# Performance work log

Measured on AMD Instinct MI355X. Metric: run time of the kernel, lower is better.

## Reference

```python
import jax, jax.numpy as jnp
import numpy as np

EPS = 1e-6  # torch.nn.CosineSimilarity eps


def _emb_sum(table, ids):
    # ids: (N, L) int -> (N, D): gather rows then sum over tokens (EmbeddingBag-sum)
    return table[ids].sum(axis=1)


def _cos_rows(q, M):
    # cosine similarity of vector q (D,) against each row of M (N, D), torch eps semantics:
    # dot / max(||a||*||b||, eps)
    num = M @ q
    den = jnp.maximum(jnp.linalg.norm(M, axis=1) * jnp.linalg.norm(q), EPS)
    return num / den


def setup_inputs() -> dict:
    key = jax.random.key(0)
    ks = jax.random.split(key, 10)
    V, D = 50000, 128
    N_MEM, N_CAND, N_PERS, L, LQ = 65536, 10000, 20, 20, 32
    return {
        "xs": jax.random.randint(ks[0], (1, LQ), 0, V, dtype=jnp.int32),
        "candidates": jax.random.randint(ks[1], (N_CAND, L), 0, V, dtype=jnp.int32),
        "persona": jax.random.randint(ks[2], (N_PERS, L), 0, V, dtype=jnp.int32),
        "keys": jax.random.randint(ks[3], (N_MEM, L), 0, V, dtype=jnp.int32),
        "values": jax.random.randint(ks[4], (N_MEM, L), 0, V, dtype=jnp.int32),
        "label": jax.random.randint(ks[5], (1, LQ), 0, V, dtype=jnp.int32),
        "shared_emb": jax.random.normal(ks[6], (V, D), dtype=jnp.float32),
        "cand_emb": jax.random.normal(ks[7], (V, D), dtype=jnp.float32),
        "R_W": jax.random.normal(ks[8], (D, D), dtype=jnp.float32) * (1.0 / np.sqrt(D)),
        "R2_W": jax.random.normal(ks[9], (D, D), dtype=jnp.float32) * (1.0 / np.sqrt(D)),
    }


def reference(xs, candidates, persona, keys, values, label, shared_emb, cand_emb, R_W, R2_W):
    enc_keys = _emb_sum(shared_emb, keys)        # (N_mem, D)
    enc_values = _emb_sum(shared_emb, values)    # (N_mem, D)
    enc_cands = _emb_sum(cand_emb, candidates)   # (N_cand, D)
    enc_pers = _emb_sum(shared_emb, persona)     # (N_pers, D)

    q = shared_emb[xs].sum(axis=1).reshape(-1)   # (D,)

    for W in (R_W, R2_W):  # loop is hardcoded to 2 hops in the source
        att = jax.nn.softmax(_cos_rows(q, enc_pers))          # (N_pers,)
        hop = (att[:, None] * enc_pers).sum(axis=0)           # (D,)
        q_plus = (q + hop) @ W.T                               # Linear no bias
        att = jax.nn.softmax(_cos_rows(q_plus, enc_keys))     # (N_mem,)
        hop = (att[:, None] * enc_values).sum(axis=0)         # (D,)
        q = (q_plus + hop) @ W.T

    preds = _cos_rows(q, enc_cands)  # (N_cand,)
    return preds
```

## Files before the change

kernel.cpp:

```cpp
#include <hip/hip_runtime.h>
#include <math.h>
#include <stdint.h>

#define D 128
#define EPS 1e-6f
typedef unsigned short u16;


__device__ __forceinline__ float wave_sum(float v) {
#pragma unroll
    for (int off = 32; off > 0; off >>= 1) v += __shfl_xor(v, off, 64);
    return v;
}
__device__ __forceinline__ float halfwave_sum(float v) {
#pragma unroll
    for (int off = 16; off > 0; off >>= 1) v += __shfl_xor(v, off, 32);
    return v;
}

__device__ __forceinline__ float bf2f(u16 h) {
    union { unsigned u; float f; } x;
    x.u = ((unsigned)h) << 16;
    return x.f;
}
__device__ __forceinline__ float bflo(unsigned u) { return bf2f((u16)(u & 0xffff)); }
__device__ __forceinline__ float bfhi(unsigned u) { return bf2f((u16)(u >> 16)); }
__device__ __forceinline__ u16 f2bf(float f) {
    union { float f; unsigned u; } x;
    x.f = f;
    unsigned u = x.u;
    return (u16)((u + 0x7fff + ((u >> 16) & 1)) >> 16);
}
__device__ __forceinline__ unsigned pack2(float a, float b) {
    return (unsigned)f2bf(a) | ((unsigned)f2bf(b) << 16);
}

__global__ void prep_k(const float* __restrict__ semb, u16* __restrict__ tbl,
                       int V, const int* __restrict__ pers, int NP,
                       const int* __restrict__ xs, int LQ,
                       float* __restrict__ enc_pers, float* __restrict__ pnorms,
                       float* __restrict__ st, int nbK) {
    const int tid = threadIdx.x;
    const int bid = blockIdx.x;
    if (bid < nbK) {
        const int n = V * 64;
        const int stride = nbK * 256;
        for (int i = bid * 256 + tid; i < n; i += stride) {
            const int v = i >> 6;
            const int c2 = i & 63;
            const float2 ab = *(const float2*)(semb + (long)v * D + 2 * c2);
            *(unsigned*)(tbl + (long)v * D + 2 * c2) = pack2(ab.x, ab.y);
        }
    } else {
        const int lane = tid & 63;
        const int half = lane >> 5;
        const int hl = lane & 31;
        const int w0 = (bid - nbK) * 4 + (tid >> 6);
        const int npr = NP + 1;
        const int npairs = (npr + 1) >> 1;
        for (int w = w0; w < npairs; w += 12) {
            const int row = 2 * w + half;
            const bool valid = row < npr;
            const int rowc = valid ? row : NP;
            const bool isq = (rowc == NP);
            const int* ids = isq ? xs : (pers + (long)rowc * 20);
            const int L = isq ? LQ : 20;
            int myid = 0;
            if (hl < L) myid = ids[hl];
            float4 acc = {0.f, 0.f, 0.f, 0.f};
            for (int t = 0; t < L; ++t) {
                const int idx = __shfl(myid, (half << 5) + t, 64);
                const float4 e = *(const float4*)(semb + (long)idx * D + 4 * hl);
                acc.x += e.x; acc.y += e.y; acc.z += e.z; acc.w += e.w;
            }
            if (valid) {
                float* outp = isq ? st : (enc_pers + (long)rowc * D);
                *(float4*)(outp + 4 * hl) = acc;
                float sq = acc.x * acc.x + acc.y * acc.y + acc.z * acc.z + acc.w * acc.w;
                sq = halfwave_sum(sq);
                if (hl == 0) {
                    if (isq) st[384] = sqrtf(sq);
                    else pnorms[rowc] = sqrtf(sq);
                }
            }
        }
    }
}

__device__ void persona_dev(const float* __restrict__ pers_rows,
                            const float* __restrict__ pnorms,
                            const float* __restrict__ W, float* __restrict__ st,
                            int NP, float* smem, int tid) {
    float* qsh = smem;
    float* qh = smem + 128;
    float* att = smem + 256;
    float* red = smem + 320;
    if (tid < D) qsh[tid] = st[tid];
    __syncthreads();
    if (tid < NP) {
        float dot = 0.f;
        const float* pr = pers_rows + (long)tid * D;
        for (int d2 = 0; d2 < D; ++d2) dot += pr[d2] * qsh[d2];
        att[tid] = dot / fmaxf(pnorms[tid] * st[384], EPS);
    }
    __syncthreads();
    if (tid == 0) {
        float m = -1e30f;
        for (int p = 0; p < NP; ++p) m = fmaxf(m, att[p]);
        float s = 0.f;
        for (int p = 0; p < NP; ++p) { att[p] = __expf(att[p] - m); s += att[p]; }
        float inv = 1.f / s;
        for (int p = 0; p < NP; ++p) att[p] *= inv;
    }
    __syncthreads();
    if (tid < D) {
        float h = 0.f;
        for (int p = 0; p < NP; ++p) h += att[p] * pers_rows[(long)p * D + tid];
        qh[tid] = qsh[tid] + h;
    }
    __syncthreads();
    float qp = 0.f;
    if (tid < D) {
        for (int d2 = 0; d2 < D; ++d2) qp += W[(long)tid * D + d2] * qh[d2];
        st[128 + tid] = qp;
    }
    float sq = wave_sum(qp * qp);
    if ((tid & 63) == 0 && tid < 128) red[tid >> 6] = sq;
    __syncthreads();
    if (tid == 0) st[385] = sqrtf(red[0] + red[1]);
    if (tid < D) st[256 + tid] = 0.f;
    if (tid == 0) st[386] = 0.f;
}

__global__ void kvp_k(const u16* __restrict__ tbl, const int* __restrict__ kids,
                      const int* __restrict__ vids, int N,
                      u16* __restrict__ vb, float* __restrict__ knorms,
                      const float* __restrict__ enc_pers,
                      const float* __restrict__ pnorms,
                      const float* __restrict__ RW, float* __restrict__ st,
                      int NP) {
    __shared__ float smem[336];
    const int tid = threadIdx.x;
    const int bid = blockIdx.x;
    if (bid == 0) {
        persona_dev(enc_pers, pnorms, RW, st, NP, smem, tid);
        return;
    }
    const int lane = tid & 63;
    const int half = lane >> 5;
    const int hl = lane & 31;
    const int ghw = ((bid - 1) * 256 + tid) >> 5;
    const int nhw = ((gridDim.x - 1) * 256) >> 5;
    for (int i = ghw; i < N; i += nhw) {
        int kid = 0, vid = 0;
        if (hl < 20) {
            kid = kids[(long)i * 20 + hl];
            vid = vids[(long)i * 20 + hl];
        }
        float k0 = 0.f, k1 = 0.f, k2 = 0.f, k3 = 0.f;
        float v0 = 0.f, v1 = 0.f, v2 = 0.f, v3 = 0.f;
#pragma unroll
        for (int t = 0; t < 20; ++t) {
            const int kj = __shfl(kid, (half << 5) + t, 64);
            const int vj = __shfl(vid, (half << 5) + t, 64);
            const ushort4 ke = *(const ushort4*)(tbl + (long)kj * D + 4 * hl);
            const ushort4 ve = *(const ushort4*)(tbl + (long)vj * D + 4 * hl);
            k0 += bf2f(ke.x); k1 += bf2f(ke.y); k2 += bf2f(ke.z); k3 += bf2f(ke.w);
            v0 += bf2f(ve.x); v1 += bf2f(ve.y); v2 += bf2f(ve.z); v3 += bf2f(ve.w);
        }
        uint2 pv;
        pv.x = pack2(v0, v1);
        pv.y = pack2(v2, v3);
        *(uint2*)(vb + (long)i * D + 4 * hl) = pv;
        float sq = halfwave_sum(k0 * k0 + k1 * k1 + k2 * k2 + k3 * k3);
        if (hl == 0) knorms[i] = sqrtf(sq);
    }
}

__global__ void a2_k(const u16* __restrict__ tbl, const float* __restrict__ st,
                     float* __restrict__ s, int V) {
    const int lane = threadIdx.x & 63;
    const float2 qp2 = *(const float2*)(st + 128 + 2 * lane);
    const int gw = (int)((blockIdx.x * blockDim.x + threadIdx.x) >> 6);
    const int nw = (int)((gridDim.x * blockDim.x) >> 6);
    for (int v = gw; v < V; v += nw) {
        const unsigned u = *(const unsigned*)(tbl + (long)v * D + 2 * lane);
        float d = bflo(u) * qp2.x + bfhi(u) * qp2.y;
        d = wave_sum(d);
        if (lane == 0) s[v] = d;
    }
}

__global__ void attcv_k(const float* __restrict__ sv, const int* __restrict__ kids,
                        const float* __restrict__ knorms, const u16* __restrict__ vb,
                        float* __restrict__ st, int N) {
    __shared__ float smem[129];
    const int tid = threadIdx.x;
    const int lane = tid & 63;
    const int half = lane >> 5;
    const int hl = lane & 31;
    const float qpn = st[385];
    const int ghw = (int)((blockIdx.x * blockDim.x + tid) >> 5);
    const int nhw = (int)((gridDim.x * blockDim.x) >> 5);
    float a0 = 0.f, a1 = 0.f, a2 = 0.f, a3 = 0.f;
    float esum = 0.f;
    for (int i = ghw; i < N; i += nhw) {
        float partial = 0.f;
        if (hl < 20) partial = sv[kids[(long)i * 20 + hl]];
        const float dot = halfwave_sum(partial);
        const float c = dot / fmaxf(knorms[i] * qpn, EPS);
        const float e = __expf(c);
        const uint2 vh = *(const uint2*)(vb + (long)i * D + 4 * hl);
        a0 += e * bflo(vh.x);
        a1 += e * bfhi(vh.x);
        a2 += e * bflo(vh.y);
        a3 += e * bfhi(vh.y);
        if (hl == 0) esum += e;
    }
    a0 += __shfl_xor(a0, 32, 64);
    a1 += __shfl_xor(a1, 32, 64);
    a2 += __shfl_xor(a2, 32, 64);
    a3 += __shfl_xor(a3, 32, 64);
    esum += __shfl_xor(esum, 32, 64);
    if (tid < 129) smem[tid] = 0.f;
    __syncthreads();
    if (half == 0) {
        atomicAdd(&smem[4 * hl + 0], a0);
        atomicAdd(&smem[4 * hl + 1], a1);
        atomicAdd(&smem[4 * hl + 2], a2);
        atomicAdd(&smem[4 * hl + 3], a3);
        if (hl == 0) atomicAdd(&smem[128], esum);
    }
    __syncthreads();
    if (tid < 128) atomicAdd(&st[256 + tid], smem[tid]);
    if (tid == 128) atomicAdd(&st[386], smem[128]);
}

__global__ void mid_hop(const float* __restrict__ W1, const float* __restrict__ W2,
                        const float* __restrict__ pers_rows,
                        const float* __restrict__ pnorms,
                        float* __restrict__ st, int NP) {
    __shared__ float qh[D];
    __shared__ float qsh[D];
    __shared__ float att[64];
    __shared__ float red[2];
    int tid = threadIdx.x;
    float inv = 1.f / st[386];
    qh[tid] = st[128 + tid] + st[256 + tid] * inv;
    __syncthreads();
    float qn = 0.f;
    for (int d2 = 0; d2 < D; ++d2) qn += W1[tid * D + d2] * qh[d2];
    qsh[tid] = qn;
    st[tid] = qn;
    float sq = wave_sum(qn * qn);
    if ((tid & 63) == 0) red[tid >> 6] = sq;
    __syncthreads();
    float qnorm = sqrtf(red[0] + red[1]);
    if (tid == 0) st[384] = qnorm;
    if (tid < NP) {
        float dot = 0.f;
        for (int d2 = 0; d2 < D; ++d2) dot += pers_rows[tid * D + d2] * qsh[d2];
        att[tid] = dot / fmaxf(pnorms[tid] * qnorm, EPS);
    }
    __syncthreads();
    if (tid == 0) {
        float m = -1e30f;
        for (int p = 0; p < NP; ++p) m = fmaxf(m, att[p]);
        float s = 0.f;
        for (int p = 0; p < NP; ++p) { att[p] = __expf(att[p] - m); s += att[p]; }
        float is = 1.f / s;
        for (int p = 0; p < NP; ++p) att[p] *= is;
    }
    __syncthreads();
    float h = 0.f;
    for (int p = 0; p < NP; ++p) h += att[p] * pers_rows[p * D + tid];
    qh[tid] = qsh[tid] + h;
    __syncthreads();
    float qp = 0.f;
    for (int d2 = 0; d2 < D; ++d2) qp += W2[tid * D + d2] * qh[d2];
    st[128 + tid] = qp;
    float sq2 = wave_sum(qp * qp);
    if ((tid & 63) == 0) red[tid >> 6] = sq2;
    __syncthreads();
    if (tid == 0) st[385] = sqrtf(red[0] + red[1]);
    st[256 + tid] = 0.f;
    if (tid == 0) st[386] = 0.f;
}

__global__ void k5f(const float* __restrict__ W2, const float* __restrict__ cemb,
                    const int* __restrict__ cands, int NC,
                    const float* __restrict__ st, float* __restrict__ out) {
    __shared__ float qv[D];
    __shared__ float qhsh[D];
    __shared__ float red[2];
    __shared__ float qns;
    const int tid = threadIdx.x;
    const float inv = 1.f / st[386];
    if (tid < D) qhsh[tid] = st[128 + tid] + st[256 + tid] * inv;
    __syncthreads();
    float qn = 0.f;
    if (tid < D) {
        for (int d2 = 0; d2 < D; ++d2) qn += W2[(long)tid * D + d2] * qhsh[d2];
        qv[tid] = qn;
    }
    float sq = wave_sum(qn * qn);
    if ((tid & 63) == 0 && tid < 128) red[tid >> 6] = sq;
    __syncthreads();
    if (tid == 0) qns = sqrtf(red[0] + red[1]);
    __syncthreads();
    const int lane = tid & 63;
    const int half = lane >> 5;
    const int hl = lane & 31;
    const int gw = (int)((blockIdx.x * blockDim.x + tid) >> 6);
    const int nw = (int)((gridDim.x * blockDim.x) >> 6);
    const float4 q4 = *(const float4*)(qv + 4 * hl);
    const float qnf = qns;
    const int npair = (NC + 1) >> 1;
    for (int p = gw; p < npair; p += nw) {
        const int row = 2 * p + half;
        const bool valid = row < NC;
        const int rowc = valid ? row : (NC - 1);
        int myid = 0;
        if (hl < 20) myid = cands[(long)rowc * 20 + hl];
        float4 acc = {0.f, 0.f, 0.f, 0.f};
#pragma unroll
        for (int t = 0; t < 20; ++t) {
            const int idx = __shfl(myid, (half << 5) + t, 64);
            const float4 e = *(const float4*)(cemb + (long)idx * D + 4 * hl);
            acc.x += e.x; acc.y += e.y; acc.z += e.z; acc.w += e.w;
        }
        float dot = halfwave_sum(acc.x * q4.x + acc.y * q4.y +
                                 acc.z * q4.z + acc.w * q4.w);
        float nsq = halfwave_sum(acc.x * acc.x + acc.y * acc.y +
                                 acc.z * acc.z + acc.w * acc.w);
        if (valid && hl == 0) out[row] = dot / fmaxf(sqrtf(nsq) * qnf, EPS);
    }
}

__global__ void encode_small_p(const float* __restrict__ emb,
                               const int* __restrict__ pers, int NP, int LP,
                               const int* __restrict__ xs, int LQ,
                               float* __restrict__ pers_rows,
                               float* __restrict__ pnorms,
                               float* __restrict__ st) {
    const int lane = threadIdx.x & 63;
    const int half = lane >> 5;
    const int hl = lane & 31;
    int gw = (int)((blockIdx.x * blockDim.x + threadIdx.x) >> 6);
    int nw = (int)((gridDim.x * blockDim.x) >> 6);
    const int npr = NP + 1;
    const int npairs = (npr + 1) >> 1;
    for (int p = gw; p < npairs; p += nw) {
        const int row = 2 * p + half;
        const bool valid = row < npr;
        const int rowc = valid ? row : NP;
        const bool isq = (rowc == NP);
        const int* ids = isq ? xs : (pers + (long)rowc * LP);
        const int L = isq ? LQ : LP;
        int myid = 0;
        if (hl < L) myid = ids[hl];
        float4 acc = {0.f, 0.f, 0.f, 0.f};
        for (int t = 0; t < L; ++t) {
            const int idx = __shfl(myid, (half << 5) + t, 64);
            const float4 e = *(const float4*)(emb + (long)idx * D + 4 * hl);
            acc.x += e.x; acc.y += e.y; acc.z += e.z; acc.w += e.w;
        }
        if (valid) {
            float* outp = isq ? st : (pers_rows + (long)rowc * D);
            *(float4*)(outp + 4 * hl) = acc;
            float sq = acc.x * acc.x + acc.y * acc.y + acc.z * acc.z + acc.w * acc.w;
            sq = halfwave_sum(sq);
            if (hl == 0) {
                if (isq) st[384] = sqrtf(sq);
                else pnorms[rowc] = sqrtf(sq);
            }
        }
    }
}

__global__ void persona_hop(const float* __restrict__ pers_rows,
                            const float* __restrict__ pnorms,
                            const float* __restrict__ W,
                            float* __restrict__ st, int NP) {
    __shared__ float smem[336];
    persona_dev(pers_rows, pnorms, W, st, NP, smem, (int)threadIdx.x);
}

__global__ void finish_hop(const float* __restrict__ W, float* __restrict__ st) {
    __shared__ float qh[D];
    __shared__ float red[2];
    int tid = threadIdx.x;
    float inv = 1.f / st[386];
    qh[tid] = st[128 + tid] + st[256 + tid] * inv;
    __syncthreads();
    float qn = 0.f;
    for (int d2 = 0; d2 < D; ++d2) qn += W[tid * D + d2] * qh[d2];
    st[tid] = qn;
    float sq = wave_sum(qn * qn);
    if ((tid & 63) == 0) red[tid >> 6] = sq;
    __syncthreads();
    if (tid == 0) st[384] = sqrtf(red[0] + red[1]);
}

__global__ void k5_final(const float* __restrict__ cemb,
                         const int* __restrict__ cands, int NC,
                         const float* __restrict__ st, float* __restrict__ out) {
    const int lane = threadIdx.x & 63;
    const int half = lane >> 5;
    const int hl = lane & 31;
    const int gw = (int)((blockIdx.x * blockDim.x + threadIdx.x) >> 6);
    const int nw = (int)((gridDim.x * blockDim.x) >> 6);
    const float4 q4 = *(const float4*)(st + 4 * hl);
    const float qn = st[384];
    const int npair = (NC + 1) >> 1;
    for (int p = gw; p < npair; p += nw) {
        const int row = 2 * p + half;
        const bool valid = row < NC;
        const int rowc = valid ? row : (NC - 1);
        int myid = 0;
        if (hl < 20) myid = cands[(long)rowc * 20 + hl];
        float4 acc = {0.f, 0.f, 0.f, 0.f};
#pragma unroll
        for (int t = 0; t < 20; ++t) {
            const int idx = __shfl(myid, (half << 5) + t, 64);
            const float4 e = *(const float4*)(cemb + (long)idx * D + 4 * hl);
            acc.x += e.x; acc.y += e.y; acc.z += e.z; acc.w += e.w;
        }
        float dot = halfwave_sum(acc.x * q4.x + acc.y * q4.y +
                                 acc.z * q4.z + acc.w * q4.w);
        float nsq = halfwave_sum(acc.x * acc.x + acc.y * acc.y +
                                 acc.z * acc.z + acc.w * acc.w);
        if (valid && hl == 0) out[row] = dot / fmaxf(sqrtf(nsq) * qn, EPS);
    }
}

__global__ void big_att_rc(const float* __restrict__ emb,
                           const int* __restrict__ kids,
                           const int* __restrict__ vids,
                           float* __restrict__ st, int N) {
    __shared__ float s[129];
    const int tid = threadIdx.x;
    const int lane = tid & 63;
    const int half = lane >> 5;
    const int hl = lane & 31;
    const int gw = (int)((blockIdx.x * blockDim.x + tid) >> 6);
    const int nw = (int)((gridDim.x * blockDim.x) >> 6);
    const float4 qp = *(const float4*)(st + 128 + 4 * hl);
    const float qpn = st[385];
    float4 hacc = {0.f, 0.f, 0.f, 0.f};
    float esum = 0.f;
    const int npair = (N + 1) >> 1;
    for (int p = gw; p < npair; p += nw) {
        const int row = 2 * p + half;
        const bool valid = row < N;
        const int rowc = valid ? row : (N - 1);
        int kid = 0, vid = 0;
        if (hl < 20) {
            kid = kids[(long)rowc * 20 + hl];
            vid = vids[(long)rowc * 20 + hl];
        }
        float4 ka = {0.f, 0.f, 0.f, 0.f}, va = {0.f, 0.f, 0.f, 0.f};
#pragma unroll
        for (int t = 0; t < 20; ++t) {
            const int ki = __shfl(kid, (half << 5) + t, 64);
            const int vi = __shfl(vid, (half << 5) + t, 64);
            const float4 ke = *(const float4*)(emb + (long)ki * D + 4 * hl);
            const float4 ve = *(const float4*)(emb + (long)vi * D + 4 * hl);
            ka.x += ke.x; ka.y += ke.y; ka.z += ke.z; ka.w += ke.w;
            va.x += ve.x; va.y += ve.y; va.z += ve.z; va.w += ve.w;
        }
        float nsq = halfwave_sum(ka.x * ka.x + ka.y * ka.y + ka.z * ka.z + ka.w * ka.w);
        float dot = halfwave_sum(ka.x * qp.x + ka.y * qp.y + ka.z * qp.z + ka.w * qp.w);
        const float c = dot / fmaxf(sqrtf(nsq) * qpn, EPS);
        float e = __expf(c);
        if (!valid) e = 0.f;
        hacc.x += e * va.x; hacc.y += e * va.y;
        hacc.z += e * va.z; hacc.w += e * va.w;
        if (hl == 0) esum += e;
    }
    hacc.x += __shfl_xor(hacc.x, 32, 64);
    hacc.y += __shfl_xor(hacc.y, 32, 64);
    hacc.z += __shfl_xor(hacc.z, 32, 64);
    hacc.w += __shfl_xor(hacc.w, 32, 64);
    esum += __shfl_xor(esum, 32, 64);
    if (tid < 129) s[tid] = 0.f;
    __syncthreads();
    if (half == 0) {
        atomicAdd(&s[4 * hl + 0], hacc.x);
        atomicAdd(&s[4 * hl + 1], hacc.y);
        atomicAdd(&s[4 * hl + 2], hacc.z);
        atomicAdd(&s[4 * hl + 3], hacc.w);
        if (hl == 0) atomicAdd(&s[128], esum);
    }
    __syncthreads();
    if (tid < 128) atomicAdd(&st[256 + tid], s[tid]);
    if (tid == 128) atomicAdd(&st[386], s[128]);
}

static inline size_t align16(size_t b) { return (b + 15) & ~(size_t)15; }

extern "C" void kernel_launch(void* const* d_in, const int* in_sizes, int n_in,
                              void* d_out, int out_size, void* d_ws, size_t ws_size,
                              hipStream_t stream) {
    const int* xs = (const int*)d_in[0];
    const int* cands = (const int*)d_in[1];
    const int* pers = (const int*)d_in[2];
    const int* keys = (const int*)d_in[3];
    const int* values = (const int*)d_in[4];
    const float* semb = (const float*)d_in[6];
    const float* cemb = (const float*)d_in[7];
    const float* RW = (const float*)d_in[8];
    const float* R2W = (const float*)d_in[9];
    float* out = (float*)d_out;

    const int L = 20;
    const int LQ = in_sizes[0];
    const int VD = in_sizes[6];
    const int V = VD / D;
    const int NMEM = in_sizes[3] / L;
    const int NCAND = in_sizes[1] / L;
    const int NPERS = in_sizes[2] / L;

    size_t need = align16((size_t)VD * 2) + align16((size_t)NMEM * D * 2) +
                  align16((size_t)NMEM * 4) * 2 + align16((size_t)V * 4) +
                  align16((size_t)NPERS * D * 4) + align16((size_t)NPERS * 4) +
                  512 * 4;
    bool stored = (d_ws != nullptr) && (ws_size >= need) && (NMEM % 4 == 0) &&
                  ((VD & 3) == 0) && (LQ <= 32);

    const int THR = 256;
    char* base = (char*)d_ws;
    u16 *tbl16 = nullptr, *vb = nullptr;
    float *knorms = nullptr, *sv = nullptr;
    if (stored) {
        tbl16 = (u16*)base;  base += align16((size_t)VD * 2);
        vb = (u16*)base;     base += align16((size_t)NMEM * D * 2);
        knorms = (float*)base; base += align16((size_t)NMEM * 4);
        base += align16((size_t)NMEM * 4);
        sv = (float*)base;   base += align16((size_t)V * 4);
    }
    float* enc_pers = (float*)base; base += align16((size_t)NPERS * D * 4);
    float* pnorms = (float*)base;   base += align16((size_t)NPERS * 4);
    float* st = (float*)base;

    if (stored) {
        const int nbK = 2048;
        prep_k<<<nbK + 3, THR, 0, stream>>>(semb, tbl16, V, pers, NPERS, xs, LQ,
                                            enc_pers, pnorms, st, nbK);
        kvp_k<<<2048, THR, 0, stream>>>(tbl16, keys, values, NMEM, vb, knorms,
                                        enc_pers, pnorms, RW, st, NPERS);
        a2_k<<<2048, THR, 0, stream>>>(tbl16, st, sv, V);
        attcv_k<<<1024, THR, 0, stream>>>(sv, keys, knorms, vb, st, NMEM);
        mid_hop<<<1, 128, 0, stream>>>(RW, R2W, enc_pers, pnorms, st, NPERS);
        a2_k<<<2048, THR, 0, stream>>>(tbl16, st, sv, V);
        attcv_k<<<1024, THR, 0, stream>>>(sv, keys, knorms, vb, st, NMEM);
        int nblk5 = (((NCAND + 1) / 2) + 3) / 4;
        k5f<<<nblk5, THR, 0, stream>>>(R2W, cemb, cands, NCAND, st, out);
        (void)n_in; (void)out_size;
        return;
    }

    {
        int npairs = (NPERS + 2) / 2;
        int blocks = (npairs + 3) / 4;
        encode_small_p<<<blocks, THR, 0, stream>>>(semb, pers, NPERS, L, xs,
                                                   LQ, enc_pers, pnorms, st);
    }
    persona_hop<<<1, 128, 0, stream>>>(enc_pers, pnorms, RW, st, NPERS);
    big_att_rc<<<1024, THR, 0, stream>>>(semb, keys, values, st, NMEM);
    mid_hop<<<1, 128, 0, stream>>>(RW, R2W, enc_pers, pnorms, st, NPERS);
    big_att_rc<<<1024, THR, 0, stream>>>(semb, keys, values, st, NMEM);
    finish_hop<<<1, 128, 0, stream>>>(R2W, st);
    int nblk5 = (((NCAND + 1) / 2) + 3) / 4;
    k5_final<<<nblk5, THR, 0, stream>>>(cemb, cands, NCAND, st, out);

    (void)n_in; (void)out_size;
}
```

Before: 313.9 us.

## Slice key/value bag encoding into 32-column chunks with sliced value layout

Replaces the key/value EmbeddingBag kernel with one where each wave processes groups of four memory rows, each quarter-wave handling a row and iterating over four 32-column slices of the bf16 table. Encoded values are stored in a slice-major layout (slice, row, 32 columns), and the attention-accumulate kernel reads that layout to match. Each wave handles two groups to add memory-level parallelism, and the persona block moves to the last block index. The aim is to improve gather locality and coalescing of table reads, at the cost of more shuffles per token and a layout tied to NMEM <= 65536.

```diff
diff --git a/kernel.cpp b/kernel.cpp
--- a/kernel.cpp
+++ b/kernel.cpp
@@ -15,6 +15,11 @@
 __device__ __forceinline__ float halfwave_sum(float v) {
 #pragma unroll
     for (int off = 16; off > 0; off >>= 1) v += __shfl_xor(v, off, 32);
+    return v;
+}
+__device__ __forceinline__ float quarter_sum(float v) {
+#pragma unroll
+    for (int off = 8; off > 0; off >>= 1) v += __shfl_xor(v, off, 16);
     return v;
 }
 
@@ -39,12 +44,12 @@
                        int V, const int* __restrict__ pers, int NP,
                        const int* __restrict__ xs, int LQ,
                        float* __restrict__ enc_pers, float* __restrict__ pnorms,
-                       float* __restrict__ st, int nbK) {
+                       float* __restrict__ st, int nbA) {
     const int tid = threadIdx.x;
     const int bid = blockIdx.x;
-    if (bid < nbK) {
+    if (bid < nbA) {
         const int n = V * 64;
-        const int stride = nbK * 256;
+        const int stride = nbA * 256;
         for (int i = bid * 256 + tid; i < n; i += stride) {
             const int v = i >> 6;
             const int c2 = i & 63;
@@ -55,7 +60,7 @@
         const int lane = tid & 63;
         const int half = lane >> 5;
         const int hl = lane & 31;
-        const int w0 = (bid - nbK) * 4 + (tid >> 6);
+        const int w0 = (bid - nbA) * 4 + (tid >> 6);
         const int npr = NP + 1;
         const int npairs = (npr + 1) >> 1;
         for (int w = w0; w < npairs; w += 12) {
@@ -132,48 +137,78 @@
     if (tid == 0) st[386] = 0.f;
 }
 
-__global__ void kvp_k(const u16* __restrict__ tbl, const int* __restrict__ kids,
-                      const int* __restrict__ vids, int N,
-                      u16* __restrict__ vb, float* __restrict__ knorms,
-                      const float* __restrict__ enc_pers,
-                      const float* __restrict__ pnorms,
-                      const float* __restrict__ RW, float* __restrict__ st,
-                      int NP) {
+__device__ __forceinline__ float kv_slice_group(
+    const u16* __restrict__ tbl, int s, int q, int ql, int kA, int kB,
+    int vA, int vB, u16* __restrict__ vb, int N, int g) {
+    float k0 = 0.f, k1 = 0.f, v0 = 0.f, v1 = 0.f;
+#pragma unroll
+    for (int t = 0; t < 20; ++t) {
+        const int j = 20 * q + t;
+        const int jb = j - 64;
+        const int ka = __shfl(kA, j & 63, 64);
+        const int kb = __shfl(kB, jb < 0 ? 0 : jb, 64);
+        const int va = __shfl(vA, j & 63, 64);
+        const int vbr = __shfl(vB, jb < 0 ? 0 : jb, 64);
+        const int kj = (j < 64) ? ka : kb;
+        const int vj = (j < 64) ? va : vbr;
+        const unsigned ke = *(const unsigned*)(tbl + (long)kj * D + 32 * s + 2 * ql);
+        const unsigned ve = *(const unsigned*)(tbl + (long)vj * D + 32 * s + 2 * ql);
+        k0 += bflo(ke); k1 += bfhi(ke);
+        v0 += bflo(ve); v1 += bfhi(ve);
+    }
+    const int row = 4 * g + q;
+    *(unsigned*)(vb + ((long)s * N + row) * 32 + 2 * ql) = pack2(v0, v1);
+    return k0 * k0 + k1 * k1;
+}
+
+__global__ void kv_all(const u16* __restrict__ tbl, const int* __restrict__ kids,
+                       const int* __restrict__ vids, int N,
+                       u16* __restrict__ vb, float* __restrict__ knorms,
+                       const float* __restrict__ enc_pers,
+                       const float* __restrict__ pnorms,
+                       const float* __restrict__ RW, float* __restrict__ st,
+                       int NP) {
     __shared__ float smem[336];
     const int tid = threadIdx.x;
     const int bid = blockIdx.x;
-    if (bid == 0) {
+    const int nbKV = gridDim.x - 1;
+    if (bid == nbKV) {
         persona_dev(enc_pers, pnorms, RW, st, NP, smem, tid);
         return;
     }
     const int lane = tid & 63;
-    const int half = lane >> 5;
-    const int hl = lane & 31;
-    const int ghw = ((bid - 1) * 256 + tid) >> 5;
-    const int nhw = ((gridDim.x - 1) * 256) >> 5;
-    for (int i = ghw; i < N; i += nhw) {
-        int kid = 0, vid = 0;
-        if (hl < 20) {
-            kid = kids[(long)i * 20 + hl];
-            vid = vids[(long)i * 20 + hl];
-        }
-        float k0 = 0.f, k1 = 0.f, k2 = 0.f, k3 = 0.f;
-        float v0 = 0.f, v1 = 0.f, v2 = 0.f, v3 = 0.f;
-#pragma unroll
-        for (int t = 0; t < 20; ++t) {
-            const int kj = __shfl(kid, (half << 5) + t, 64);
-            const int vj = __shfl(vid, (half << 5) + t, 64);
-            const ushort4 ke = *(const ushort4*)(tbl + (long)kj * D + 4 * hl);
-            const ushort4 ve = *(const ushort4*)(tbl + (long)vj * D + 4 * hl);
-            k0 += bf2f(ke.x); k1 += bf2f(ke.y); k2 += bf2f(ke.z); k3 += bf2f(ke.w);
-            v0 += bf2f(ve.x); v1 += bf2f(ve.y); v2 += bf2f(ve.z); v3 += bf2f(ve.w);
-        }
-        uint2 pv;
-        pv.x = pack2(v0, v1);
-        pv.y = pack2(v2, v3);
-        *(uint2*)(vb + (long)i * D + 4 * hl) = pv;
-        float sq = halfwave_sum(k0 * k0 + k1 * k1 + k2 * k2 + k3 * k3);
-        if (hl == 0) knorms[i] = sqrtf(sq);
+    const int q = lane >> 4;
+    const int ql = lane & 15;
+    const int w = bid * 4 + (tid >> 6);
+    const int nwaves = nbKV * 4;
+    const int ngroup = N >> 2;
+    const int g0 = w;
+    const int g1 = w + nwaves;
+    int kA0 = 0, kB0 = 0, vA0 = 0, vB0 = 0;
+    int kA1 = 0, kB1 = 0, vA1 = 0, vB1 = 0;
+    if (g0 < ngroup) {
+        const long ib = (long)g0 * 80;
+        kA0 = kids[ib + lane]; vA0 = vids[ib + lane];
+        if (lane < 16) { kB0 = kids[ib + 64 + lane]; vB0 = vids[ib + 64 + lane]; }
+    }
+    if (g1 < ngroup) {
+        const long ib = (long)g1 * 80;
+        kA1 = kids[ib + lane]; vA1 = vids[ib + lane];
+        if (lane < 16) { kB1 = kids[ib + 64 + lane]; vB1 = vids[ib + 64 + lane]; }
+    }
+    float sq0 = 0.f, sq1 = 0.f;
+#pragma unroll
+    for (int s = 0; s < 4; ++s) {
+        if (g0 < ngroup) sq0 += kv_slice_group(tbl, s, q, ql, kA0, kB0, vA0, vB0, vb, N, g0);
+        if (g1 < ngroup) sq1 += kv_slice_group(tbl, s, q, ql, kA1, kB1, vA1, vB1, vb, N, g1);
+    }
+    if (g0 < ngroup) {
+        const float sq = quarter_sum(sq0);
+        if (ql == 0) knorms[4 * g0 + q] = sqrtf(sq);
+    }
+    if (g1 < ngroup) {
+        const float sq = quarter_sum(sq1);
+        if (ql == 0) knorms[4 * g1 + q] = sqrtf(sq);
     }
 }
 
@@ -199,6 +234,8 @@
     const int lane = tid & 63;
     const int half = lane >> 5;
     const int hl = lane & 31;
+    const int s4 = hl >> 3;
+    const int w8 = hl & 7;
     const float qpn = st[385];
     const int ghw = (int)((blockIdx.x * blockDim.x + tid) >> 5);
     const int nhw = (int)((gridDim.x * blockDim.x) >> 5);
@@ -210,11 +247,11 @@
         const float dot = halfwave_sum(partial);
         const float c = dot / fmaxf(knorms[i] * qpn, EPS);
         const float e = __expf(c);
-        const uint2 vh = *(const uint2*)(vb + (long)i * D + 4 * hl);
-        a0 += e * bflo(vh.x);
-        a1 += e * bfhi(vh.x);
-        a2 += e * bflo(vh.y);
-        a3 += e * bfhi(vh.y);
+        const ushort4 vh = *(const ushort4*)(vb + ((long)s4 * N + i) * 32 + 4 * w8);
+        a0 += e * bf2f(vh.x);
+        a1 += e * bf2f(vh.y);
+        a2 += e * bf2f(vh.z);
+        a3 += e * bf2f(vh.w);
         if (hl == 0) esum += e;
     }
     a0 += __shfl_xor(a0, 32, 64);
@@ -225,10 +262,11 @@
     if (tid < 129) smem[tid] = 0.f;
     __syncthreads();
     if (half == 0) {
-        atomicAdd(&smem[4 * hl + 0], a0);
-        atomicAdd(&smem[4 * hl + 1], a1);
-        atomicAdd(&smem[4 * hl + 2], a2);
-        atomicAdd(&smem[4 * hl + 3], a3);
+        const int ch = 32 * s4 + 4 * w8;
+        atomicAdd(&smem[ch + 0], a0);
+        atomicAdd(&smem[ch + 1], a1);
+        atomicAdd(&smem[ch + 2], a2);
+        atomicAdd(&smem[ch + 3], a3);
         if (hl == 0) atomicAdd(&smem[128], esum);
     }
     __syncthreads();
@@ -522,11 +560,11 @@
     const int NPERS = in_sizes[2] / L;
 
     size_t need = align16((size_t)VD * 2) + align16((size_t)NMEM * D * 2) +
-                  align16((size_t)NMEM * 4) * 2 + align16((size_t)V * 4) +
+                  align16((size_t)NMEM * 4) + align16((size_t)V * 4) +
                   align16((size_t)NPERS * D * 4) + align16((size_t)NPERS * 4) +
                   512 * 4;
     bool stored = (d_ws != nullptr) && (ws_size >= need) && (NMEM % 4 == 0) &&
-                  ((VD & 3) == 0) && (LQ <= 32);
+                  (NMEM <= 65536) && ((VD & 3) == 0) && (LQ <= 32);
 
     const int THR = 256;
     char* base = (char*)d_ws;
@@ -536,7 +574,6 @@
         tbl16 = (u16*)base;  base += align16((size_t)VD * 2);
         vb = (u16*)base;     base += align16((size_t)NMEM * D * 2);
         knorms = (float*)base; base += align16((size_t)NMEM * 4);
-        base += align16((size_t)NMEM * 4);
         sv = (float*)base;   base += align16((size_t)V * 4);
     }
     float* enc_pers = (float*)base; base += align16((size_t)NPERS * D * 4);
@@ -544,11 +581,11 @@
     float* st = (float*)base;
 
     if (stored) {
-        const int nbK = 2048;
-        prep_k<<<nbK + 3, THR, 0, stream>>>(semb, tbl16, V, pers, NPERS, xs, LQ,
-                                            enc_pers, pnorms, st, nbK);
-        kvp_k<<<2048, THR, 0, stream>>>(tbl16, keys, values, NMEM, vb, knorms,
-                                        enc_pers, pnorms, RW, st, NPERS);
+        const int nbA = 2048;
+        prep_k<<<nbA + 3, THR, 0, stream>>>(semb, tbl16, V, pers, NPERS, xs, LQ,
+                                            enc_pers, pnorms, st, nbA);
+        kv_all<<<2049, THR, 0, stream>>>(tbl16, keys, values, NMEM, vb, knorms,
+                                         enc_pers, pnorms, RW, st, NPERS);
         a2_k<<<2048, THR, 0, stream>>>(tbl16, st, sv, V);
         attcv_k<<<1024, THR, 0, stream>>>(sv, keys, knorms, vb, st, NMEM);
         mid_hop<<<1, 128, 0, stream>>>(RW, R2W, enc_pers, pnorms, st, NPERS);
```

New measurement: 349.4 us. 11.3% more time.

## Partition key/value gathers into four vocabulary ranges to improve cache locality

Applied to the files above, without the earlier changes.

The key/value embedding gather loop in kvp_k now makes four passes over the token list. Each pass loads only the table rows whose ids fall in one quarter of the vocabulary, aiming to keep concurrent gathers within a smaller, cache-resident slice of the bf16 table. The cost is four times the shuffles and predicate checks, divergent branches, and a changed summation order. The launch also adds one block to kvp_k, removes an unused workspace slot, and adds an NMEM limit to the stored-path condition.

```diff
diff --git a/kernel.cpp b/kernel.cpp
--- a/kernel.cpp
+++ b/kernel.cpp
@@ -39,12 +39,12 @@
                        int V, const int* __restrict__ pers, int NP,
                        const int* __restrict__ xs, int LQ,
                        float* __restrict__ enc_pers, float* __restrict__ pnorms,
-                       float* __restrict__ st, int nbK) {
+                       float* __restrict__ st, int nbA) {
     const int tid = threadIdx.x;
     const int bid = blockIdx.x;
-    if (bid < nbK) {
+    if (bid < nbA) {
         const int n = V * 64;
-        const int stride = nbK * 256;
+        const int stride = nbA * 256;
         for (int i = bid * 256 + tid; i < n; i += stride) {
             const int v = i >> 6;
             const int c2 = i & 63;
@@ -55,7 +55,7 @@
         const int lane = tid & 63;
         const int half = lane >> 5;
         const int hl = lane & 31;
-        const int w0 = (bid - nbK) * 4 + (tid >> 6);
+        const int w0 = (bid - nbA) * 4 + (tid >> 6);
         const int npr = NP + 1;
         const int npairs = (npr + 1) >> 1;
         for (int w = w0; w < npairs; w += 12) {
@@ -133,7 +133,7 @@
 }
 
 __global__ void kvp_k(const u16* __restrict__ tbl, const int* __restrict__ kids,
-                      const int* __restrict__ vids, int N,
+                      const int* __restrict__ vids, int N, int V,
                       u16* __restrict__ vb, float* __restrict__ knorms,
                       const float* __restrict__ enc_pers,
                       const float* __restrict__ pnorms,
@@ -160,13 +160,24 @@
         float k0 = 0.f, k1 = 0.f, k2 = 0.f, k3 = 0.f;
         float v0 = 0.f, v1 = 0.f, v2 = 0.f, v3 = 0.f;
 #pragma unroll
-        for (int t = 0; t < 20; ++t) {
-            const int kj = __shfl(kid, (half << 5) + t, 64);
-            const int vj = __shfl(vid, (half << 5) + t, 64);
-            const ushort4 ke = *(const ushort4*)(tbl + (long)kj * D + 4 * hl);
-            const ushort4 ve = *(const ushort4*)(tbl + (long)vj * D + 4 * hl);
-            k0 += bf2f(ke.x); k1 += bf2f(ke.y); k2 += bf2f(ke.z); k3 += bf2f(ke.w);
-            v0 += bf2f(ve.x); v1 += bf2f(ve.y); v2 += bf2f(ve.z); v3 += bf2f(ve.w);
+        for (int c = 0; c < 4; ++c) {
+            const int lo = (int)(((long)c * V) >> 2);
+            const int hi = (c == 3) ? V : (int)(((long)(c + 1) * V) >> 2);
+#pragma unroll
+            for (int t = 0; t < 20; ++t) {
+                const int kj = __shfl(kid, (half << 5) + t, 64);
+                const int vj = __shfl(vid, (half << 5) + t, 64);
+                if (kj >= lo && kj < hi) {
+                    const ushort4 ke = *(const ushort4*)(tbl + (long)kj * D + 4 * hl);
+                    k0 += bf2f(ke.x); k1 += bf2f(ke.y);
+                    k2 += bf2f(ke.z); k3 += bf2f(ke.w);
+                }
+                if (vj >= lo && vj < hi) {
+                    const ushort4 ve = *(const ushort4*)(tbl + (long)vj * D + 4 * hl);
+                    v0 += bf2f(ve.x); v1 += bf2f(ve.y);
+                    v2 += bf2f(ve.z); v3 += bf2f(ve.w);
+                }
+            }
         }
         uint2 pv;
         pv.x = pack2(v0, v1);
@@ -522,11 +533,11 @@
     const int NPERS = in_sizes[2] / L;
 
     size_t need = align16((size_t)VD * 2) + align16((size_t)NMEM * D * 2) +
-                  align16((size_t)NMEM * 4) * 2 + align16((size_t)V * 4) +
+                  align16((size_t)NMEM * 4) + align16((size_t)V * 4) +
                   align16((size_t)NPERS * D * 4) + align16((size_t)NPERS * 4) +
                   512 * 4;
     bool stored = (d_ws != nullptr) && (ws_size >= need) && (NMEM % 4 == 0) &&
-                  ((VD & 3) == 0) && (LQ <= 32);
+                  (NMEM <= 65536) && ((VD & 3) == 0) && (LQ <= 32);
 
     const int THR = 256;
     char* base = (char*)d_ws;
@@ -536,7 +547,6 @@
         tbl16 = (u16*)base;  base += align16((size_t)VD * 2);
         vb = (u16*)base;     base += align16((size_t)NMEM * D * 2);
         knorms = (float*)base; base += align16((size_t)NMEM * 4);
-        base += align16((size_t)NMEM * 4);
         sv = (float*)base;   base += align16((size_t)V * 4);
     }
     float* enc_pers = (float*)base; base += align16((size_t)NPERS * D * 4);
@@ -544,11 +554,11 @@
     float* st = (float*)base;
 
     if (stored) {
-        const int nbK = 2048;
-        prep_k<<<nbK + 3, THR, 0, stream>>>(semb, tbl16, V, pers, NPERS, xs, LQ,
-                                            enc_pers, pnorms, st, nbK);
-        kvp_k<<<2048, THR, 0, stream>>>(tbl16, keys, values, NMEM, vb, knorms,
-                                        enc_pers, pnorms, RW, st, NPERS);
+        const int nbA = 2048;
+        prep_k<<<nbA + 3, THR, 0, stream>>>(semb, tbl16, V, pers, NPERS, xs, LQ,
+                                            enc_pers, pnorms, st, nbA);
+        kvp_k<<<2049, THR, 0, stream>>>(tbl16, keys, values, NMEM, V, vb,
+                                        knorms, enc_pers, pnorms, RW, st, NPERS);
         a2_k<<<2048, THR, 0, stream>>>(tbl16, st, sv, V);
         attcv_k<<<1024, THR, 0, stream>>>(sv, keys, knorms, vb, st, NMEM);
         mid_hop<<<1, 128, 0, stream>>>(RW, R2W, enc_pers, pnorms, st, NPERS);
```

After: 377.4 us. 1.2x slower.
